# Kernel optimization log

Hardware: AMD Instinct MI355X
Metric: run time of the kernel (lower is better)

Reference implementation:

```python
import jax, jax.numpy as jnp
import numpy as np
from jax.ops import segment_sum

N_NODES = 50000
N_EDGES = 50000
N_GRAPHS = 1024


def _inv_deg(idx, num_segments):
    deg = segment_sum(jnp.ones(idx.shape[0], jnp.float32), idx, num_segments=num_segments)
    return jnp.where(deg > 0, 1.0 / deg, 0.0)


def hypergraph_conv(x, W, b, node_idx, edge_idx):
    # PyG HypergraphConv (use_attention=False, heads=1, hyperedge_weight=1):
    # out = D^{-1} H B^{-1} H^T (X W) + b
    D = _inv_deg(node_idx, N_NODES)   # inverse node degree [N]
    B = _inv_deg(edge_idx, N_EDGES)   # inverse hyperedge degree [E]
    xl = x @ W                         # [N, out]
    # node -> hyperedge aggregation
    edge_feat = B[:, None] * segment_sum(xl[node_idx], edge_idx, num_segments=N_EDGES)
    # hyperedge -> node aggregation
    out = D[:, None] * segment_sum(edge_feat[edge_idx], node_idx, num_segments=N_NODES)
    return out + b


def global_mean_pool(x, batch):
    s = segment_sum(x, batch, num_segments=N_GRAPHS)
    cnt = segment_sum(jnp.ones(x.shape[0], jnp.float32), batch, num_segments=N_GRAPHS)
    return s / jnp.maximum(cnt, 1.0)[:, None]


def setup_inputs() -> dict:
    key = jax.random.key(0)
    ks = jax.random.split(key, 16)
    F, H = 128, 256
    def lin(k, fi, fo):
        s = 1.0 / np.sqrt(fi)
        k1, k2 = jax.random.split(k)
        return (jax.random.uniform(k1, (fi, fo), jnp.float32, -s, s),
                jax.random.uniform(k2, (fo,), jnp.float32, -s, s))
    W1, b1 = lin(ks[0], F, H)
    W2, b2 = lin(ks[1], H, 2 * H)
    W3, b3 = lin(ks[2], 2 * H, H)
    Wl1, bl1 = lin(ks[3], H, H // 2)
    Wl2, bl2 = lin(ks[4], H // 2, 1)
    x = jax.random.normal(ks[5], (N_NODES, F), jnp.float32)
    hyperedge_index = jax.random.randint(ks[6], (2, 400000), 0, N_EDGES, jnp.int64)
    batch = jnp.sort(jax.random.randint(ks[7], (N_NODES,), 0, N_GRAPHS, jnp.int64))
    return {"x": x, "hyperedge_index": hyperedge_index, "batch": batch,
            "W1": W1, "b1": b1, "W2": W2, "b2": b2, "W3": W3, "b3": b3,
            "Wl1": Wl1, "bl1": bl1, "Wl2": Wl2, "bl2": bl2}


def reference(x, hyperedge_index, batch, W1, b1, W2, b2, W3, b3, Wl1, bl1, Wl2, bl2):
    node_idx, edge_idx = hyperedge_index[0], hyperedge_index[1]
    h = jax.nn.relu(hypergraph_conv(x, W1, b1, node_idx, edge_idx))
    h = jax.nn.relu(hypergraph_conv(h, W2, b2, node_idx, edge_idx))
    h = jax.nn.relu(hypergraph_conv(h, W3, b3, node_idx, edge_idx))
    g = global_mean_pool(h, batch)              # [G, H]
    g = jax.nn.relu(g @ Wl1 + bl1)
    out = g @ Wl2 + bl2                          # [G, 1]
    return out
```

## Files before the change

### kernel.cpp

```cpp
#include <hip/hip_runtime.h>
#include <hip/hip_bf16.h>

#define N_NODES  50000
#define N_EDGES  50000
#define N_INC    400000
#define N_GRAPHS 1024
#define M_PAD    50048
#define SEG_CAP  50176

typedef __bf16 bf16x8 __attribute__((ext_vector_type(8)));
typedef float  f32x4  __attribute__((ext_vector_type(4)));

__device__ __forceinline__ unsigned short f2bf(float f) {
    __hip_bfloat16 h = __float2bfloat16(f);
    return __builtin_bit_cast(unsigned short, h);
}
__device__ __forceinline__ float bflo(unsigned int u) {
    return __builtin_bit_cast(float, u << 16);
}
__device__ __forceinline__ float bfhi(unsigned int u) {
    return __builtin_bit_cast(float, u & 0xffff0000u);
}
__device__ __forceinline__ unsigned int packbf(float a, float b) {
    return (unsigned int)f2bf(a) | ((unsigned int)f2bf(b) << 16);
}
__device__ __forceinline__ void load_lds16(const unsigned short* g, unsigned short* l) {
    __builtin_amdgcn_global_load_lds((const __attribute__((address_space(1))) void*)g,
                                     (__attribute__((address_space(3))) void*)l, 16, 0, 0);
}

#define NB_INC  1563
__global__ __launch_bounds__(256) void normhist_kernel(const int* __restrict__ hei,
                                                       int* __restrict__ nidx, int* __restrict__ eidx,
                                                       unsigned short* __restrict__ rn,
                                                       unsigned short* __restrict__ re,
                                                       int* __restrict__ ndeg_p, int* __restrict__ edeg_p) {
    __shared__ int s32;
    int t = threadIdx.x;
    if (t == 0) s32 = 0;
    __syncthreads();
    int probe = hei[4 * t + 1] | hei[4 * t + 3];
    if (probe) s32 = 1;
    __syncthreads();
    int is32 = s32;
    int i = blockIdx.x * 256 + t;
    if (i < N_INC) {
        int n, e;
        if (is32) { n = hei[i];     e = hei[N_INC + i]; }
        else      { n = hei[2 * i]; e = hei[2 * N_INC + 2 * i]; }
        nidx[i] = n; eidx[i] = e;
        rn[i] = (unsigned short)atomicAdd(&ndeg_p[n << 4], 1);
        re[i] = (unsigned short)atomicAdd(&edeg_p[e << 4], 1);
    }
}

__global__ __launch_bounds__(256) void scan_up_f(const int* __restrict__ edeg_p,
                                                 const int* __restrict__ ndeg_p,
                                                 const int* __restrict__ hei,
                                                 const int* __restrict__ braw,
                                                 int* __restrict__ eoff, int* __restrict__ noff,
                                                 int* __restrict__ goff,
                                                 int* __restrict__ partials) {
    int b = blockIdx.x, t = threadIdx.x;
    if (b >= 98) {
        __shared__ int s32;
        if (t == 0) s32 = 0;
        __syncthreads();
        int probe = hei[4 * t + 1] | hei[4 * t + 3];
        if (probe) s32 = 1;
        __syncthreads();
        int is32 = s32;
        int g = (b - 98) * 256 + t;
        int lo = 0, hi = N_NODES;
        while (lo < hi) {
            int mid = (lo + hi) >> 1;
            int v = is32 ? braw[mid] : braw[2 * mid];
            if (v < g) lo = mid + 1; else hi = mid;
        }
        goff[g] = lo;
        if (g == 1023) goff[1024] = N_NODES;
        return;
    }
    __shared__ int lds[256];
    const int* in; int* outp; int lb;
    if (b < 49) { in = edeg_p; outp = eoff; lb = b; }
    else        { in = ndeg_p; outp = noff; lb = b - 49; }
    int base = lb * 1024 + t * 4;
    int4 v;
    v.x = in[(size_t)(base + 0) << 4];
    v.y = in[(size_t)(base + 1) << 4];
    v.z = in[(size_t)(base + 2) << 4];
    v.w = in[(size_t)(base + 3) << 4];
    int s = v.x + v.y + v.z + v.w;
    lds[t] = s;
    __syncthreads();
    for (int off = 1; off < 256; off <<= 1) {
        int u = (t >= off) ? lds[t - off] : 0;
        __syncthreads();
        lds[t] += u;
        __syncthreads();
    }
    int excl = lds[t] - s;
    if (t == 255) partials[b] = lds[255];
    int4 o;
    o.x = excl;
    o.y = excl + v.x;
    o.z = o.y + v.y;
    o.w = o.z + v.z;
    *(int4*)(outp + base) = o;
}

__global__ __launch_bounds__(256) void scan_down_f(int* __restrict__ eoff,
                                                   int* __restrict__ noff,
                                                   const int* __restrict__ partials) {
    __shared__ int lds[98];
    int b = blockIdx.x, t = threadIdx.x;
    if (t < 98) lds[t] = partials[t];
    __syncthreads();
    if (t < 2) {
        int lo = t * 49, hi = lo + 49;
        int run = 0;
        for (int i = lo; i < hi; ++i) { int x = lds[i]; lds[i] = run; run += x; }
    }
    __syncthreads();
    int* outp; int lb;
    if (b < 49) { outp = eoff; lb = b; }
    else        { outp = noff; lb = b - 49; }
    int base = lb * 1024 + t * 4;
    int p = lds[b];
    int4 v = *(const int4*)(outp + base);
    v.x += p; v.y += p; v.z += p; v.w += p;
    *(int4*)(outp + base) = v;
}

#define NB_CSR  1563
#define NB_CONV 6250
#define NB_W1   128
#define NB_W2   512
#define NB_W3   512
__global__ __launch_bounds__(256) void prep_kernel(const int* __restrict__ nidx,
                                                   const int* __restrict__ eidx,
                                                   const unsigned short* __restrict__ rn,
                                                   const unsigned short* __restrict__ re,
                                                   const int* __restrict__ eoff,
                                                   const int* __restrict__ noff,
                                                   unsigned short* __restrict__ csre,
                                                   unsigned short* __restrict__ csrn,
                                                   const float* __restrict__ x,
                                                   unsigned short* __restrict__ xbf,
                                                   const float* __restrict__ W1, unsigned short* __restrict__ wt1,
                                                   const float* __restrict__ W2, unsigned short* __restrict__ wt2,
                                                   const float* __restrict__ W3, unsigned short* __restrict__ wt3) {
    int b = blockIdx.x, t = threadIdx.x;
    if (b < NB_CSR) {
        int i = b * 256 + t;
        if (i < N_INC) {
            int n = nidx[i], e = eidx[i];
            csre[eoff[e] + re[i]] = (unsigned short)n;
            csrn[noff[n] + rn[i]] = (unsigned short)e;
        }
    } else if (b < NB_CSR + NB_CONV) {
        int i = (b - NB_CSR) * 256 + t;
        float4 v = *(const float4*)(x + 4 * (size_t)i);
        ushort4 o;
        o.x = f2bf(v.x); o.y = f2bf(v.y); o.z = f2bf(v.z); o.w = f2bf(v.w);
        *(ushort4*)(xbf + 4 * (size_t)i) = o;
    } else if (b < NB_CSR + NB_CONV + NB_W1) {
        int i = (b - NB_CSR - NB_CONV) * 256 + t;
        int k = i >> 8, n = i & 255;
        wt1[n * 128 + k] = f2bf(W1[i]);
    } else if (b < NB_CSR + NB_CONV + NB_W1 + NB_W2) {
        int i = (b - NB_CSR - NB_CONV - NB_W1) * 256 + t;
        int k = i >> 9, n = i & 511;
        wt2[n * 256 + k] = f2bf(W2[i]);
    } else {
        int i = (b - NB_CSR - NB_CONV - NB_W1 - NB_W2) * 256 + t;
        int k = i >> 8, n = i & 255;
        wt3[n * 512 + k] = f2bf(W3[i]);
    }
}

template <bool EPI>
__global__ __launch_bounds__(256) void gemm128_kernel(const unsigned short* __restrict__ A,
                                                      const unsigned short* __restrict__ Bt,
                                                      const float* __restrict__ bias,
                                                      unsigned short* __restrict__ C,
                                                      int M, int K, int N) {
    __shared__ unsigned short As[128 * 32];
    __shared__ unsigned short Bs[128 * 32];
    __shared__ unsigned short Cs[32][140];
    int tid  = threadIdx.x;
    int wave = tid >> 6, lane = tid & 63;
    int n0 = blockIdx.x * 128, m0 = blockIdx.y * 128;
    int quad = lane >> 4, fr = lane & 15;
    int wr = wave >> 1, wc = wave & 1;
    int lrow16 = lane >> 2;
    int lchunk = (lane & 3) * 8;

    const unsigned short* gsrc;
    unsigned short* ldst;
    if (wave < 2) { gsrc = A  + (size_t)(m0 + wave * 64) * K;       ldst = As + wave * 64 * 32; }
    else          { gsrc = Bt + (size_t)(n0 + (wave - 2) * 64) * K; ldst = Bs + (wave - 2) * 64 * 32; }

    f32x4 acc[4][4];
#pragma unroll
    for (int s = 0; s < 4; ++s)
#pragma unroll
        for (int c = 0; c < 4; ++c) acc[s][c] = (f32x4){0.f, 0.f, 0.f, 0.f};

    for (int k0 = 0; k0 < K; k0 += 32) {
#pragma unroll
        for (int l = 0; l < 4; ++l) {
            const unsigned short* g = gsrc + (size_t)(l * 16 + lrow16) * K + k0 + lchunk;
            load_lds16(g, ldst + l * 16 * 32);
        }
        __syncthreads();
        bf16x8 af[4], bfr[4];
#pragma unroll
        for (int s = 0; s < 4; ++s)
            af[s] = *(const bf16x8*)&As[(wr * 64 + s * 16 + fr) * 32 + quad * 8];
#pragma unroll
        for (int c = 0; c < 4; ++c)
            bfr[c] = *(const bf16x8*)&Bs[(wc * 64 + c * 16 + fr) * 32 + quad * 8];
#pragma unroll
        for (int s = 0; s < 4; ++s)
#pragma unroll
            for (int c = 0; c < 4; ++c)
                acc[s][c] = __builtin_amdgcn_mfma_f32_16x16x32_bf16(af[s], bfr[c], acc[s][c], 0, 0, 0);
        __syncthreads();
    }

    float bv[4];
#pragma unroll
    for (int c = 0; c < 4; ++c) bv[c] = EPI ? bias[n0 + wc * 64 + c * 16 + fr] : 0.f;
#pragma unroll
    for (int s = 0; s < 4; ++s) {
#pragma unroll
        for (int c = 0; c < 4; ++c)
#pragma unroll
            for (int r = 0; r < 4; ++r) {
                float v = acc[s][c][r];
                if (EPI) v = fmaxf(v + bv[c], 0.f);
                Cs[wr * 16 + quad * 4 + r][wc * 64 + c * 16 + fr] = f2bf(v);
            }
        __syncthreads();
#pragma unroll
        for (int i = 0; i < 2; ++i) {
            int rl  = i * 16 + (tid >> 4);
            int col = (tid & 15) * 8;
            int gm  = m0 + (rl >> 4) * 64 + s * 16 + (rl & 15);
            if (gm < M) {
                uint4 v = *(const uint4*)&Cs[rl][col];
                *(uint4*)&C[(size_t)gm * N + n0 + col] = v;
            }
        }
        __syncthreads();
    }
}

template <int C, bool BIAS>
__device__ __forceinline__ void seg_bodyN(const unsigned short* __restrict__ in,
                                          const int* __restrict__ offs,
                                          const int* __restrict__ degs_p,
                                          const unsigned short* __restrict__ csr_src,
                                          const float* __restrict__ bias,
                                          unsigned short* __restrict__ outp,
                                          int nseg) {
    constexpr int LPG = C / 8;
    constexpr int SPW = 64 / LPG;
    int wid  = (blockIdx.x * 256 + threadIdx.x) >> 6;
    int lane = threadIdx.x & 63;
    int grp = lane / LPG, lg = lane % LPG;
    int seg = SPW * wid + grp;
    if (SPW * wid >= nseg) return;
    bool segvalid = seg < nseg;
    int deg   = segvalid ? degs_p[(size_t)seg << 4] : 0;
    int start = segvalid ? offs[seg] : 0;
    float dinv = (deg > 0) ? 1.0f / (float)deg : 0.0f;
    int maxdeg = deg;
#pragma unroll
    for (int m = LPG; m < 64; m <<= 1) maxdeg = max(maxdeg, __shfl_xor(maxdeg, m, 64));
    const unsigned short* cs = csr_src + start;
    float acc[8];
#pragma unroll
    for (int q = 0; q < 8; ++q) acc[q] = 0.f;
    size_t lbase = (size_t)lg * 8;

    auto loadrow = [&](int src, unsigned int* v) {
        src = min(src, nseg - 1);
        const unsigned int* p = (const unsigned int*)(in + (size_t)src * C + lbase);
        uint4 t = *(const uint4*)p; v[0] = t.x; v[1] = t.y; v[2] = t.z; v[3] = t.w;
    };
    auto maccum = [&](unsigned int* v, unsigned int msk) {
#pragma unroll
        for (int q = 0; q < 4; ++q) {
            unsigned int x = v[q] & msk;
            acc[2 * q] += bflo(x); acc[2 * q + 1] += bfhi(x);
        }
    };

    int dc = (deg > 0) ? deg - 1 : 0;
    for (int j = 0; j < maxdeg; j += 8) {
        unsigned int v[8][4];
        int row[8];
#pragma unroll
        for (int u = 0; u < 8; ++u) {
            int jj = min(j + u, dc);
            row[u] = (int)cs[jj];
        }
#pragma unroll
        for (int u = 0; u < 8; ++u) loadrow(row[u], v[u]);
        __asm__ __volatile__("" ::: "memory");
#pragma unroll
        for (int u = 0; u < 8; ++u) {
            unsigned int msk = (j + u < deg) ? 0xffffffffu : 0u;
            maccum(v[u], msk);
        }
    }

    if (!segvalid) return;
    unsigned int o[4];
#pragma unroll
    for (int q = 0; q < 4; ++q) {
        float a = acc[2 * q] * dinv;
        float b = acc[2 * q + 1] * dinv;
        if constexpr (BIAS) {
            a = fmaxf(a + bias[lbase + 2 * q], 0.f);
            b = fmaxf(b + bias[lbase + 2 * q + 1], 0.f);
        }
        o[q] = packbf(a, b);
    }
    *(uint4*)(outp + (size_t)seg * C + lbase) = make_uint4(o[0], o[1], o[2], o[3]);
}

template <int C>
__global__ __launch_bounds__(256) void seg_edge_t(const unsigned short* __restrict__ xl,
                                                  const int* __restrict__ eoff,
                                                  const int* __restrict__ edeg_p,
                                                  const unsigned short* __restrict__ csr_src,
                                                  unsigned short* __restrict__ ef) {
    seg_bodyN<C, false>(xl, eoff, edeg_p, csr_src, nullptr, ef, N_EDGES);
}

template <int C, bool BIAS>
__global__ __launch_bounds__(256) void seg_node_t(const unsigned short* __restrict__ ef,
                                                  const int* __restrict__ noff,
                                                  const int* __restrict__ ndeg_p,
                                                  const unsigned short* __restrict__ csr_src,
                                                  const float* __restrict__ bias,
                                                  unsigned short* __restrict__ hout) {
    seg_bodyN<C, BIAS>(ef, noff, ndeg_p, csr_src, bias, hout, N_NODES);
}

__global__ __launch_bounds__(256) void pool_head_kernel(const unsigned short* __restrict__ h,
                                                        const int* __restrict__ goff,
                                                        const float* __restrict__ Wl1,
                                                        const float* __restrict__ bl1,
                                                        const float* __restrict__ Wl2,
                                                        const float* __restrict__ bl2,
                                                        float* __restrict__ out) {
    __shared__ float xs[256];
    __shared__ float red[128];
    int g = blockIdx.x, t = threadIdx.x;
    int s = goff[g], cnt = goff[g + 1] - s;
    float acc = 0.f;
    for (int i = 0; i < cnt; ++i) {
        unsigned int u = h[(size_t)(s + i) * 256 + t];
        acc += __builtin_bit_cast(float, u << 16);
    }
    xs[t] = acc / (float)(cnt > 0 ? cnt : 1);
    __syncthreads();
    if (t < 128) {
        float s2 = 0.f;
        for (int f = 0; f < 256; ++f) s2 += xs[f] * Wl1[f * 128 + t];
        s2 = fmaxf(s2 + bl1[t], 0.f);
        red[t] = s2 * Wl2[t];
    }
    __syncthreads();
    for (int off = 64; off > 0; off >>= 1) {
        if (t < off) red[t] += red[t + off];
        __syncthreads();
    }
    if (t == 0) out[g] = red[0] + bl2[0];
}

extern "C" void kernel_launch(void* const* d_in, const int* in_sizes, int n_in,
                              void* d_out, int out_size, void* d_ws, size_t ws_size,
                              hipStream_t stream) {
    const float* x     = (const float*)d_in[0];
    const int* hei     = (const int*)d_in[1];
    const int* braw    = (const int*)d_in[2];
    const float* W1    = (const float*)d_in[3];
    const float* b1    = (const float*)d_in[4];
    const float* W2    = (const float*)d_in[5];
    const float* b2    = (const float*)d_in[6];
    const float* W3    = (const float*)d_in[7];
    const float* b3    = (const float*)d_in[8];
    const float* Wl1   = (const float*)d_in[9];
    const float* bl1   = (const float*)d_in[10];
    const float* Wl2   = (const float*)d_in[11];
    const float* bl2   = (const float*)d_in[12];
    float* out         = (float*)d_out;

    char* w = (char*)d_ws;
    size_t off = 0;
    auto alloc = [&](size_t bytes) { size_t p = off; off += (bytes + 255) & ~(size_t)255; return p; };
    size_t o_edegp = alloc((size_t)SEG_CAP * 16 * 4);
    size_t o_ndegp = alloc((size_t)SEG_CAP * 16 * 4);
    size_t zero_end = off;
    size_t o_eoff = alloc((size_t)SEG_CAP * 4);
    size_t o_noff = alloc((size_t)SEG_CAP * 4);
    size_t o_goff = alloc((size_t)1025 * 4);
    size_t o_part = alloc(128 * 4);
    size_t o_nidx = alloc((size_t)N_INC * 4);
    size_t o_eidx = alloc((size_t)N_INC * 4);
    size_t o_rn   = alloc((size_t)N_INC * 2);
    size_t o_re   = alloc((size_t)N_INC * 2);
    size_t o_csre = alloc((size_t)N_INC * 2 + 64);
    size_t o_csrn = alloc((size_t)N_INC * 2 + 64);
    size_t o_wt1  = alloc((size_t)128 * 256 * 2);
    size_t o_wt2  = alloc((size_t)256 * 512 * 2);
    size_t o_wt3  = alloc((size_t)512 * 256 * 2);
    size_t o_xbf  = alloc((size_t)M_PAD * 128 * 2);
    size_t o_Y    = alloc((size_t)M_PAD * 256 * 2);
    size_t o_H1   = alloc((size_t)M_PAD * 256 * 2);
    size_t o_H2   = alloc((size_t)M_PAD * 512 * 2);
    size_t o_bufE = alloc((size_t)N_EDGES * 256 * 2);

    int* edeg_p = (int*)(w + o_edegp);
    int* ndeg_p = (int*)(w + o_ndegp);
    int* eoff = (int*)(w + o_eoff);
    int* noff = (int*)(w + o_noff);
    int* goff = (int*)(w + o_goff);
    int* part = (int*)(w + o_part);
    int* nidx = (int*)(w + o_nidx);
    int* eidx = (int*)(w + o_eidx);
    unsigned short* rn   = (unsigned short*)(w + o_rn);
    unsigned short* re   = (unsigned short*)(w + o_re);
    unsigned short* csre = (unsigned short*)(w + o_csre);
    unsigned short* csrn = (unsigned short*)(w + o_csrn);
    unsigned short* wt1  = (unsigned short*)(w + o_wt1);
    unsigned short* wt2  = (unsigned short*)(w + o_wt2);
    unsigned short* wt3  = (unsigned short*)(w + o_wt3);
    unsigned short* xbf  = (unsigned short*)(w + o_xbf);
    unsigned short* Y    = (unsigned short*)(w + o_Y);
    unsigned short* H1   = (unsigned short*)(w + o_H1);
    unsigned short* H2   = (unsigned short*)(w + o_H2);
    unsigned short* bufE = (unsigned short*)(w + o_bufE);

    hipMemsetAsync(w, 0, zero_end, stream);
    normhist_kernel<<<NB_INC, 256, 0, stream>>>(hei, nidx, eidx, rn, re, ndeg_p, edeg_p);
    scan_up_f<<<102, 256, 0, stream>>>(edeg_p, ndeg_p, hei, braw, eoff, noff, goff, part);
    scan_down_f<<<98, 256, 0, stream>>>(eoff, noff, part);
    prep_kernel<<<NB_CSR + NB_CONV + NB_W1 + NB_W2 + NB_W3, 256, 0, stream>>>(
        nidx, eidx, rn, re, eoff, noff, csre, csrn, x, xbf, W1, wt1, W2, wt2, W3, wt3);

    int segGrid2 = ((N_NODES + 1) / 2 * 64 + 255) / 256;
    int segGrid4 = ((N_NODES + 3) / 4 * 64 + 255) / 256;

    seg_edge_t<128><<<segGrid4, 256, 0, stream>>>(xbf, eoff, edeg_p, csre, bufE);
    seg_node_t<128, false><<<segGrid4, 256, 0, stream>>>(bufE, noff, ndeg_p, csrn, nullptr, Y);
    {
        dim3 grid(256 / 128, M_PAD / 128);
        gemm128_kernel<true><<<grid, 256, 0, stream>>>(Y, wt1, b1, H1, N_NODES, 128, 256);
    }
    seg_edge_t<256><<<segGrid2, 256, 0, stream>>>(H1, eoff, edeg_p, csre, bufE);
    seg_node_t<256, false><<<segGrid2, 256, 0, stream>>>(bufE, noff, ndeg_p, csrn, nullptr, Y);
    {
        dim3 grid(512 / 128, M_PAD / 128);
        gemm128_kernel<true><<<grid, 256, 0, stream>>>(Y, wt2, b2, H2, N_NODES, 256, 512);
    }
    {
        dim3 grid(256 / 128, M_PAD / 128);
        gemm128_kernel<false><<<grid, 256, 0, stream>>>(H2, wt3, nullptr, Y, N_NODES, 512, 256);
    }
    seg_edge_t<256><<<segGrid2, 256, 0, stream>>>(Y, eoff, edeg_p, csre, bufE);
    seg_node_t<256, true><<<segGrid2, 256, 0, stream>>>(bufE, noff, ndeg_p, csrn, b3, H1);

    pool_head_kernel<<<N_GRAPHS, 256, 0, stream>>>(H1, goff, Wl1, bl1, Wl2, bl2, out);
}
```

Measured before the change: 414.0 us.

## Double GEMM K-tile to 64 with XOR-swizzled LDS and batched epilogue

The bf16 MFMA GEMM now stages a K-slice of 64 per iteration instead of 32. This halves the number of loop iterations and barrier pairs, and each staged tile feeds two MFMA k-steps. The shared-memory tile rows are XOR-swizzled on the 16-byte chunk index to avoid LDS bank conflicts on the wider row stride. The C-tile staging buffer reuses the same shared memory and writes two 16-row slices per barrier round, which reduces epilogue syncs. Shared memory per block grows, which may lower occupancy.

```diff
diff --git a/kernel.cpp b/kernel.cpp
--- a/kernel.cpp
+++ b/kernel.cpp
@@ -186,21 +186,21 @@
                                                       const float* __restrict__ bias,
                                                       unsigned short* __restrict__ C,
                                                       int M, int K, int N) {
-    __shared__ unsigned short As[128 * 32];
-    __shared__ unsigned short Bs[128 * 32];
-    __shared__ unsigned short Cs[32][140];
+    __shared__ unsigned short smem[2 * 128 * 64];
+    unsigned short* As = smem;
+    unsigned short* Bs = smem + 128 * 64;
     int tid  = threadIdx.x;
     int wave = tid >> 6, lane = tid & 63;
     int n0 = blockIdx.x * 128, m0 = blockIdx.y * 128;
     int quad = lane >> 4, fr = lane & 15;
     int wr = wave >> 1, wc = wave & 1;
-    int lrow16 = lane >> 2;
-    int lchunk = (lane & 3) * 8;
+    int lrow8 = lane >> 3;
+    int lcol  = ((lane & 7) ^ lrow8) * 8;
 
     const unsigned short* gsrc;
     unsigned short* ldst;
-    if (wave < 2) { gsrc = A  + (size_t)(m0 + wave * 64) * K;       ldst = As + wave * 64 * 32; }
-    else          { gsrc = Bt + (size_t)(n0 + (wave - 2) * 64) * K; ldst = Bs + (wave - 2) * 64 * 32; }
+    if (wave < 2) { gsrc = A  + (size_t)(m0 + wave * 64) * K;       ldst = As + wave * 64 * 64; }
+    else          { gsrc = Bt + (size_t)(n0 + (wave - 2) * 64) * K; ldst = Bs + (wave - 2) * 64 * 64; }
 
     f32x4 acc[4][4];
 #pragma unroll
@@ -208,47 +208,56 @@
 #pragma unroll
         for (int c = 0; c < 4; ++c) acc[s][c] = (f32x4){0.f, 0.f, 0.f, 0.f};
 
-    for (int k0 = 0; k0 < K; k0 += 32) {
-#pragma unroll
-        for (int l = 0; l < 4; ++l) {
-            const unsigned short* g = gsrc + (size_t)(l * 16 + lrow16) * K + k0 + lchunk;
-            load_lds16(g, ldst + l * 16 * 32);
-        }
-        __syncthreads();
-        bf16x8 af[4], bfr[4];
-#pragma unroll
-        for (int s = 0; s < 4; ++s)
-            af[s] = *(const bf16x8*)&As[(wr * 64 + s * 16 + fr) * 32 + quad * 8];
-#pragma unroll
-        for (int c = 0; c < 4; ++c)
-            bfr[c] = *(const bf16x8*)&Bs[(wc * 64 + c * 16 + fr) * 32 + quad * 8];
-#pragma unroll
-        for (int s = 0; s < 4; ++s)
+    int swz = fr & 7;
+    for (int k0 = 0; k0 < K; k0 += 64) {
+#pragma unroll
+        for (int l = 0; l < 8; ++l) {
+            const unsigned short* g = gsrc + (size_t)(l * 8 + lrow8) * K + k0 + lcol;
+            load_lds16(g, ldst + l * 8 * 64);
+        }
+        __syncthreads();
+#pragma unroll
+        for (int kk = 0; kk < 2; ++kk) {
+            int slot = (kk * 4 + quad) ^ swz;
+            bf16x8 af[4], bfr[4];
+#pragma unroll
+            for (int s = 0; s < 4; ++s)
+                af[s] = *(const bf16x8*)&As[(wr * 64 + s * 16 + fr) * 64 + slot * 8];
 #pragma unroll
             for (int c = 0; c < 4; ++c)
-                acc[s][c] = __builtin_amdgcn_mfma_f32_16x16x32_bf16(af[s], bfr[c], acc[s][c], 0, 0, 0);
+                bfr[c] = *(const bf16x8*)&Bs[(wc * 64 + c * 16 + fr) * 64 + slot * 8];
+#pragma unroll
+            for (int s = 0; s < 4; ++s)
+#pragma unroll
+                for (int c = 0; c < 4; ++c)
+                    acc[s][c] = __builtin_amdgcn_mfma_f32_16x16x32_bf16(af[s], bfr[c], acc[s][c], 0, 0, 0);
+        }
         __syncthreads();
     }
 
     float bv[4];
 #pragma unroll
     for (int c = 0; c < 4; ++c) bv[c] = EPI ? bias[n0 + wc * 64 + c * 16 + fr] : 0.f;
-#pragma unroll
-    for (int s = 0; s < 4; ++s) {
-#pragma unroll
-        for (int c = 0; c < 4; ++c)
-#pragma unroll
-            for (int r = 0; r < 4; ++r) {
-                float v = acc[s][c][r];
-                if (EPI) v = fmaxf(v + bv[c], 0.f);
-                Cs[wr * 16 + quad * 4 + r][wc * 64 + c * 16 + fr] = f2bf(v);
-            }
-        __syncthreads();
-#pragma unroll
-        for (int i = 0; i < 2; ++i) {
+    unsigned short (*Cs)[136] = reinterpret_cast<unsigned short (*)[136]>(smem);
+#pragma unroll
+    for (int sp = 0; sp < 2; ++sp) {
+#pragma unroll
+        for (int sl = 0; sl < 2; ++sl) {
+#pragma unroll
+            for (int c = 0; c < 4; ++c)
+#pragma unroll
+                for (int r = 0; r < 4; ++r) {
+                    float v = acc[sp * 2 + sl][c][r];
+                    if (EPI) v = fmaxf(v + bv[c], 0.f);
+                    Cs[sl * 32 + wr * 16 + quad * 4 + r][wc * 64 + c * 16 + fr] = f2bf(v);
+                }
+        }
+        __syncthreads();
+#pragma unroll
+        for (int i = 0; i < 4; ++i) {
             int rl  = i * 16 + (tid >> 4);
             int col = (tid & 15) * 8;
-            int gm  = m0 + (rl >> 4) * 64 + s * 16 + (rl & 15);
+            int gm  = m0 + ((rl & 31) >> 4) * 64 + (sp * 2 + (rl >> 5)) * 16 + (rl & 15);
             if (gm < M) {
                 uint4 v = *(const uint4*)&Cs[rl][col];
                 *(uint4*)&C[(size_t)gm * N + n0 + col] = v;
```

New measurement: 402.8 us. 2.7% less time.
